# Optimization experiments

Hardware: AMD Instinct MI355X
Metric: run time of the kernel (lower is better)

The kernel has to match this reference:

```python
import jax, jax.numpy as jnp
import numpy as np

B, L, D, H = 4, 1024, 1024, 16
HD = D // H
TERM = 20  # N-term / C-term window size


def setup_inputs() -> dict:
    key = jax.random.key(0)
    ks = jax.random.split(key, 9)
    x = jax.random.normal(ks[0], (B, L, D), jnp.float32)
    lens = jax.random.randint(ks[1], (B,), 64, L + 1)
    mask = jnp.arange(L)[None, :] < lens[:, None]  # contiguous valid prefix, bool [B,L]
    s = 0.02  # ~ xavier_uniform with gain 1/H**0.25
    Wq = jax.random.normal(ks[2], (D, D), jnp.float32) * s
    Wk = jax.random.normal(ks[3], (D, D), jnp.float32) * s
    Wv = jax.random.normal(ks[4], (D, D), jnp.float32) * s
    bq = jnp.zeros((D,), jnp.float32)
    bk = jnp.zeros((D,), jnp.float32)
    bv = jnp.zeros((D,), jnp.float32)
    gamma = jnp.ones((D,), jnp.float32)
    beta = jnp.zeros((D,), jnp.float32)
    return {"x": x, "mask": mask, "Wq": Wq, "bq": bq, "Wk": Wk, "bk": bk,
            "Wv": Wv, "bv": bv, "gamma": gamma, "beta": beta}


def reference(x, mask, Wq, bq, Wk, bk, Wv, bv, gamma, beta):
    # LayerNorm (eps = 1e-5, torch default)
    mu = x.mean(-1, keepdims=True)
    var = ((x - mu) ** 2).mean(-1, keepdims=True)
    xn = (x - mu) / jnp.sqrt(var + 1e-5) * gamma + beta

    Q = (xn @ Wq + bq).reshape(B, L, H, HD)
    K = (xn @ Wk + bk).reshape(B, L, H, HD)
    V = (xn @ Wv + bv).reshape(B, L, H, HD)

    # note: original divides by head_dim**0.25 (quarter power) - keep faithful
    scores = jnp.einsum('bqhd,bkhd->bhqk', Q, K) / HD ** 0.25

    # mask fill on key positions
    scores = jnp.where(mask[:, None, None, :], scores, -10000.0)

    # per-sample length-dependent bias on key positions
    lens = mask.sum(-1)                      # [B] int
    pos = jnp.arange(L)                      # [L]
    inlen = pos[None, :] < lens[:, None]     # [B,L]
    bias_ge = (1.0 * (pos[None, :] < TERM)
               + 0.8 * ((pos[None, :] >= lens[:, None] - TERM) & inlen))
    bias_lt = (1.0 + 0.8) * inlen
    bias = jnp.where((lens >= TERM)[:, None], bias_ge, bias_lt)  # [B,L]
    scores = scores + bias[:, None, None, :]

    attn = jax.nn.softmax(scores, axis=-1)   # [B,H,L,L]
    entropy_loss = -(attn * jnp.log(attn + 1e-10)).sum(-1).mean()

    context = jnp.einsum('bhqk,bkhd->bqhd', attn, V).reshape(B, L, D)

    # ragged N-term / C-term mean pooling (vectorized segment means)
    term = jnp.minimum(TERM, lens)           # [B]
    termf = term.astype(x.dtype)[:, None]
    wn = (pos[None, :] < term[:, None]).astype(x.dtype)                      # first term tokens
    wc = ((pos[None, :] >= (lens - term)[:, None]) & inlen).astype(x.dtype)  # last term valid tokens
    n_term = (context * wn[:, :, None]).sum(1) / termf
    c_term = (context * wc[:, :, None]).sum(1) / termf
    global_pool = context.mean(1)            # mean over full L, as in original

    pooled = jnp.concatenate([n_term, c_term, global_pool], axis=1)  # [B,3D]
    return pooled, attn.mean(1), entropy_loss
```

## Files before the change

kernel.cpp:

```cpp
#include <hip/hip_runtime.h>
#include <hip/hip_bf16.h>
#include <hip/hip_fp16.h>


typedef unsigned short u16;
typedef __attribute__((ext_vector_type(4))) float f32x4;
typedef __attribute__((ext_vector_type(8))) __bf16 bf16x8;
typedef __attribute__((ext_vector_type(4))) unsigned int u32x4;
typedef __attribute__((ext_vector_type(4))) unsigned short u16x4;
typedef __attribute__((ext_vector_type(8))) unsigned short u16x8;

typedef const __attribute__((address_space(1))) unsigned int* gas1;
typedef __attribute__((address_space(3))) unsigned int* las3;

#define DEV __device__ __forceinline__

DEV float bf2f(u16 u){ union{unsigned i; float f;} c; c.i = ((unsigned)u)<<16; return c.f; }
DEV u16 f2bf(float f){ union{float f; unsigned i;} c; c.f=f; unsigned i=c.i;
  unsigned r = i + 0x7FFFu + ((i>>16)&1u); return (u16)(r>>16); }

__global__ void k_detect(const void* mask, const void* gamma, const void* beta,
                         const void* bq, const void* bk, const void* bv,
                         int* lens, float* ent, int* flag,
                         u16* gam_c, u16* bet_c, u16* bq_c, u16* bk_c, u16* bv_c,
                         float* pacc){
  int t = threadIdx.x; int w = t>>6; int lane = t&63;
  int isf32 = (((const u16*)gamma)[0] == 0) ? 1 : 0;
  if (t==0){ *flag = isf32; *ent = 0.f; }
  for (int i=t; i<12288; i+=256) pacc[i] = 0.f;
  for (int i=t; i<1024; i+=256){
    if (isf32){
      gam_c[i]=f2bf(((const float*)gamma)[i]); bet_c[i]=f2bf(((const float*)beta)[i]);
      bq_c[i] =f2bf(((const float*)bq)[i]);    bk_c[i] =f2bf(((const float*)bk)[i]);
      bv_c[i] =f2bf(((const float*)bv)[i]);
    } else {
      gam_c[i]=((const u16*)gamma)[i]; bet_c[i]=((const u16*)beta)[i];
      bq_c[i] =((const u16*)bq)[i];    bk_c[i] =((const u16*)bk)[i];
      bv_c[i] =((const u16*)bv)[i];
    }
  }
  const unsigned char* mb = (const unsigned char*)mask;
  const int* mi = (const int*)mask;
  const u16* ms = (const u16*)mask;
  int cnt = 0;
  if (mb[1] != 0) {
    if (mb[0]==1 && mb[1]==1) { for (int i=lane;i<1024;i+=64) cnt += (mb[w*1024+i]!=0); }
    else                      { for (int i=lane;i<1024;i+=64) cnt += (ms[w*1024+i]!=0); }
  } else {
    if (mi[1]==0)             { for (int i=lane;i<1024;i+=64) cnt += (mi[(w*1024+i)*2]!=0); }
    else                      { for (int i=lane;i<1024;i+=64) cnt += (mi[w*1024+i]!=0); }
  }
  #pragma unroll
  for (int o=32;o;o>>=1) cnt += __shfl_down(cnt,o);
  if (lane==0) lens[w] = cnt;
}

__global__ __launch_bounds__(256) void k_ln(const void* x, const u16* gamma, const u16* beta,
                                            u16* xn, const int* flagp){
  int isf32 = *flagp;
  int row = blockIdx.x, t = threadIdx.x;
  float f0,f1,f2,f3;
  if (isf32){
    f32x4 v = ((const f32x4*)x)[(size_t)row*256 + t];
    f0=v[0]; f1=v[1]; f2=v[2]; f3=v[3];
  } else {
    u16x4 v = ((const u16x4*)x)[(size_t)row*256 + t];
    f0=bf2f(v[0]); f1=bf2f(v[1]); f2=bf2f(v[2]); f3=bf2f(v[3]);
  }
  float s = f0+f1+f2+f3;
  float sq = f0*f0+f1*f1+f2*f2+f3*f3;
  #pragma unroll
  for (int o=32;o;o>>=1){ s += __shfl_down(s,o); sq += __shfl_down(sq,o); }
  __shared__ float rs[4], rq[4];
  if ((t&63)==0){ rs[t>>6]=s; rq[t>>6]=sq; }
  __syncthreads();
  s = rs[0]+rs[1]+rs[2]+rs[3]; sq = rq[0]+rq[1]+rq[2]+rq[3];
  float mu = s*(1.0f/1024.0f);
  float var = sq*(1.0f/1024.0f) - mu*mu;
  float rstd = rsqrtf(var + 1e-5f);
  u16x4 gv = ((const u16x4*)gamma)[t];
  u16x4 bv = ((const u16x4*)beta)[t];
  u16x4 o;
  o[0]=f2bf((f0-mu)*rstd*bf2f(gv[0])+bf2f(bv[0]));
  o[1]=f2bf((f1-mu)*rstd*bf2f(gv[1])+bf2f(bv[1]));
  o[2]=f2bf((f2-mu)*rstd*bf2f(gv[2])+bf2f(bv[2]));
  o[3]=f2bf((f3-mu)*rstd*bf2f(gv[3])+bf2f(bv[3]));
  ((u16x4*)(xn + (size_t)row*1024))[t] = o;
}

DEV void tr64_body(const void* src, u16* dst, int R, int C, int bt, int isf32, int t,
                   u16 (*tile)[68]){
  int tc_n = C>>6;
  int tr = (bt / tc_n)<<6, tc = (bt % tc_n)<<6;
  if (isf32){
    const float* s = (const float*)src;
    #pragma unroll
    for (int it=0; it<2; ++it){
      int f = it*2048 + t*8; int r=f>>6, c=f&63;
      const float* p = s + (long)(tr+r)*C + tc + c;
      f32x4 a = *(const f32x4*)p, b = *(const f32x4*)(p+4);
      u16x4 ua, ub;
      #pragma unroll
      for (int j=0;j<4;j++){ ua[j]=f2bf(a[j]); ub[j]=f2bf(b[j]); }
      *(u16x4*)&tile[r][c]   = ua;
      *(u16x4*)&tile[r][c+4] = ub;
    }
  } else {
    const u16* s = (const u16*)src;
    #pragma unroll
    for (int it=0; it<2; ++it){
      int f = it*2048 + t*8; int r=f>>6, c=f&63;
      *(u16x4*)&tile[r][c]   = *(const u16x4*)(s + (long)(tr+r)*C + tc + c);
      *(u16x4*)&tile[r][c+4] = *(const u16x4*)(s + (long)(tr+r)*C + tc + c + 4);
    }
  }
  __syncthreads();
  #pragma unroll
  for (int it=0; it<2; ++it){
    int f = it*2048 + t*8; int r=f>>6, c=f&63;
    u16x4 a, b2;
    #pragma unroll
    for (int j=0;j<4;j++){ a[j]=tile[c+j][r]; b2[j]=tile[c+4+j][r]; }
    *(u16x4*)(dst + (long)(tc+r)*R + tr + c)     = a;
    *(u16x4*)(dst + (long)(tc+r)*R + tr + c + 4) = b2;
  }
}

__global__ __launch_bounds__(256) void k_trW(const void* Wq, const void* Wk, const void* Wv,
                                             u16* Wt, const int* flagp){
  __shared__ u16 tile[64][68];
  int isf32 = *flagp;
  const void* src = (blockIdx.y==0) ? Wq : (blockIdx.y==1) ? Wk : Wv;
  u16* dst = Wt + ((size_t)blockIdx.y<<20);
  tr64_body(src, dst, 1024, 1024, blockIdx.x, isf32, threadIdx.x, tile);
}

__global__ __launch_bounds__(256) void k_trV(const u16* Vb, u16* Vt){
  __shared__ u16 tile[64][68];
  tr64_body(Vb + ((size_t)blockIdx.y<<16), Vt + ((size_t)blockIdx.y<<16),
            1024, 64, blockIdx.x, 0, threadIdx.x, tile);
}

__global__ __launch_bounds__(256) void k_gemm(const u16* A, const u16* Bt,
    const u16* biasq, const u16* biask, const u16* biasv,
    u16* Qb, u16* Kb, u16* Vb){
  __shared__ u16 lA[2][4096];
  __shared__ u16 lB[2][4096];
  int t = threadIdx.x;
  int w = t>>6, l = t&63, g = l>>4, lc = l&15;
  int wm = w>>1, wn = w&1;
  int m0 = (blockIdx.x & 31)<<7;
  int n0 = (int)(blockIdx.x >> 5)<<7;
  int fb0 = t*16, fb1 = 4096 + t*16;
  int r0 = fb0>>6, c0 = fb0&63, r1 = fb1>>6, c1 = fb1&63;
  const char* Ab = (const char*)A; const char* Bb = (const char*)Bt;
  long aoff0 = (long)(m0+r0)*2048 + c0;
  long aoff1 = (long)(m0+r1)*2048 + c1;
  long boff0 = (long)(n0+r0)*2048 + c0;
  long boff1 = (long)(n0+r1)*2048 + c1;
  int lw = w<<10;

  #define STAGEK(buf, ko) do{ \
    __builtin_amdgcn_global_load_lds((gas1)(const void*)(Ab + aoff0 + (ko)), \
        (las3)(void*)((char*)&lA[buf][0] + lw), 16, 0, 0); \
    __builtin_amdgcn_global_load_lds((gas1)(const void*)(Ab + aoff1 + (ko)), \
        (las3)(void*)((char*)&lA[buf][0] + 4096 + lw), 16, 0, 0); \
    __builtin_amdgcn_global_load_lds((gas1)(const void*)(Bb + boff0 + (ko)), \
        (las3)(void*)((char*)&lB[buf][0] + lw), 16, 0, 0); \
    __builtin_amdgcn_global_load_lds((gas1)(const void*)(Bb + boff1 + (ko)), \
        (las3)(void*)((char*)&lB[buf][0] + 4096 + lw), 16, 0, 0); \
  }while(0)

  f32x4 vzero = {0.f,0.f,0.f,0.f};
  f32x4 acc[4][4];
  #pragma unroll
  for (int i=0;i<4;i++)
    #pragma unroll
    for (int j=0;j<4;j++) acc[i][j] = vzero;

  STAGEK(0, 0);
  __syncthreads();
  for (int kt=0; kt<32; ++kt){
    int cur = kt & 1;
    if (kt < 31) STAGEK(cur^1, (long)(kt+1)*64);
    bf16x8 af[4], bfr[4];
    #pragma unroll
    for (int i=0;i<4;i++) af[i]  = *(const bf16x8*)(const void*)&lA[cur][((wm<<6)+(i<<4)+lc)*32 + (g<<3)];
    #pragma unroll
    for (int j=0;j<4;j++) bfr[j] = *(const bf16x8*)(const void*)&lB[cur][((wn<<6)+(j<<4)+lc)*32 + (g<<3)];
    #pragma unroll
    for (int i=0;i<4;i++)
      #pragma unroll
      for (int j=0;j<4;j++)
        acc[i][j] = __builtin_amdgcn_mfma_f32_16x16x32_bf16(af[i], bfr[j], acc[i][j], 0,0,0);
    __syncthreads();
  }
  #undef STAGEK
  #pragma unroll
  for (int j=0;j<4;j++){
    int n = n0 + (wn<<6) + (j<<4) + lc;
    int kind = n>>10; int nn = n & 1023;
    const u16* bp = (kind==0)?biasq:(kind==1)?biask:biasv;
    float bvl = bf2f(bp[nn]);
    u16* dst = (kind==0)?Qb:(kind==1)?Kb:Vb;
    int h = nn>>6, hd = n&63;
    #pragma unroll
    for (int i=0;i<4;i++){
      #pragma unroll
      for (int r=0;r<4;r++){
        int m = m0 + (wm<<6) + (i<<4) + (g<<2) + r;
        int bb = m>>10, pos = m&1023;
        dst[(((bb<<4)+h)<<16) + (pos<<6) + hd] = f2bf(acc[i][j][r] + bvl);
      }
    }
  }
}

__global__ __launch_bounds__(512) void k_attn(const u16* Qg, const u16* Kg, const u16* Vt,
    const int* lens, u16* ctx, u16* Pp, float* ent_acc){
  __shared__ u16 Plds[16][1032];
  __shared__ float redz[16][8];
  __shared__ float rede[16][8];
  __shared__ __half redc[2][16][66];
  int bqi = blockIdx.x;
  int qt = bqi & 63, hg = (bqi>>6)&3, b = bqi>>8;
  int q0 = qt<<4;
  int t = threadIdx.x, w = t>>6, l = t&63, g = l>>4, lc = l&15;
  int kh = w>>2, dg = w&3;
  int len = lens[b];
  {
    u16x8 z8 = {0,0,0,0,0,0,0,0};
    u16* pz = &Plds[0][0];
    for (int i=t; i<2064; i+=512) *(u16x8*)(pz + i*8) = z8;
  }
  __half2 mh[8][2];
  #pragma unroll
  for (int i=0;i<8;i++){ mh[i][0] = __float2half2_rn(0.f); mh[i][1] = __float2half2_rn(0.f); }
  float ent_local = 0.f;
  const float SCALE = 0.35355339059327373f;
  for (int hh=0; hh<4; ++hh){
    int h = (hg<<2) + hh;
    int base = ((b<<4)+h)<<16;
    bf16x8 qf0 = *(const bf16x8*)(const void*)(Qg + base + ((q0+lc)<<6) + (g<<3));
    bf16x8 qf1 = *(const bf16x8*)(const void*)(Qg + base + ((q0+lc)<<6) + (g<<3) + 32);
    f32x4 s[8];
    float zp[4]={0,0,0,0}, ep[4]={0,0,0,0};
    #pragma unroll
    for (int tt=0; tt<8; ++tt){
      int kb = (tt<<7)+(w<<4);
      if (kb < len){
        const u16* kp = Kg + base + ((kb+lc)<<6) + (g<<3);
        bf16x8 kf0 = *(const bf16x8*)(const void*)kp;
        bf16x8 kf1 = *(const bf16x8*)(const void*)(kp + 32);
        f32x4 a = {0.f,0.f,0.f,0.f};
        a = __builtin_amdgcn_mfma_f32_16x16x32_bf16(qf0, kf0, a, 0,0,0);
        a = __builtin_amdgcn_mfma_f32_16x16x32_bf16(qf1, kf1, a, 0,0,0);
        int key = kb + lc;
        bool valid = key < len;
        float bias;
        if (len >= 20) bias = (key<20 ? 1.0f : 0.0f) + ((valid && key >= len-20) ? 0.8f : 0.0f);
        else bias = 1.8f;
        #pragma unroll
        for (int r=0;r<4;r++){
          float sv = valid ? a[r]*SCALE + bias : -10000.0f;
          float e = __expf(fminf(sv, 60.0f));
          zp[r]+=e; ep[r]+=e*sv;
          a[r] = e;
          Plds[(g<<2)+r][key] = f2bf(e);
        }
        s[tt] = a;
      }
    }
    #pragma unroll
    for (int r=0;r<4;r++){
      zp[r]+=__shfl_xor(zp[r],1); ep[r]+=__shfl_xor(ep[r],1);
      zp[r]+=__shfl_xor(zp[r],2); ep[r]+=__shfl_xor(ep[r],2);
      zp[r]+=__shfl_xor(zp[r],4); ep[r]+=__shfl_xor(ep[r],4);
      zp[r]+=__shfl_xor(zp[r],8); ep[r]+=__shfl_xor(ep[r],8);
    }
    if (lc==0){
      #pragma unroll
      for (int r=0;r<4;r++){ redz[(g<<2)+r][w]=zp[r]; rede[(g<<2)+r][w]=ep[r]; }
    }
    __syncthreads();
    float invz[4];
    #pragma unroll
    for (int r=0;r<4;r++){
      int rr=(g<<2)+r;
      float Z = redz[rr][0]+redz[rr][1]+redz[rr][2]+redz[rr][3]
              + redz[rr][4]+redz[rr][5]+redz[rr][6]+redz[rr][7];
      float E = rede[rr][0]+rede[rr][1]+rede[rr][2]+rede[rr][3]
              + rede[rr][4]+rede[rr][5]+rede[rr][6]+rede[rr][7];
      invz[r] = 1.0f/Z;
      if (w==0 && lc==0) ent_local += __logf(Z) - E*invz[r];
    }
    #pragma unroll
    for (int tt=0;tt<8;++tt){
      if (((tt<<7)+(w<<4)) < len){
        float p0 = s[tt][0]*invz[0], p1 = s[tt][1]*invz[1];
        float p2 = s[tt][2]*invz[2], p3 = s[tt][3]*invz[3];
        mh[tt][0] = __hadd2(mh[tt][0], __halves2half2(__float2half_rn(p0), __float2half_rn(p1)));
        mh[tt][1] = __hadd2(mh[tt][1], __halves2half2(__float2half_rn(p2), __float2half_rn(p3)));
      }
    }
    f32x4 cacc = {0.f,0.f,0.f,0.f};
    const u16* vrow = Vt + base + (((dg<<4)+lc)<<10);
    #pragma unroll
    for (int ks=0; ks<16; ++ks){
      int kk = (ks<<1)+kh;
      if ((kk<<5) < len){
        bf16x8 pa = *(const bf16x8*)(const void*)(&Plds[0][0] + lc*1032 + (kk<<5) + (g<<3));
        bf16x8 vb = *(const bf16x8*)(const void*)(vrow + (kk<<5) + (g<<3));
        cacc = __builtin_amdgcn_mfma_f32_16x16x32_bf16(pa, vb, cacc, 0,0,0);
      }
    }
    #pragma unroll
    for (int r=0;r<4;r++) redc[kh][(g<<2)+r][(dg<<4)+lc] = __float2half(cacc[r]*invz[r]);
    __syncthreads();
    #pragma unroll
    for (int ii=0; ii<2; ++ii){
      int i = t + (ii<<9);
      int q = i>>6, d = i&63;
      float v = __half2float(redc[0][q][d]) + __half2float(redc[1][q][d]);
      ctx[(((size_t)(b<<10)+q0+q)<<10) + (h<<6) + d] = f2bf(v);
    }
  }
  u16* oa = Pp + ((size_t)hg<<22) + ((size_t)b<<20);
  #pragma unroll
  for (int tt=0; tt<8; ++tt){
    int col = (tt<<7)+(w<<4)+lc;
    int qb_ = (q0+(g<<2))<<10;
    oa[qb_ + col]            = __half_as_ushort(__low2half(mh[tt][0]));
    oa[qb_ + 1024 + col]     = __half_as_ushort(__high2half(mh[tt][0]));
    oa[qb_ + 2048 + col]     = __half_as_ushort(__low2half(mh[tt][1]));
    oa[qb_ + 3072 + col]     = __half_as_ushort(__high2half(mh[tt][1]));
  }
  if (w==0){
    float es = ent_local;
    #pragma unroll
    for (int o=32;o;o>>=1) es += __shfl_down(es,o);
    if (l==0) atomicAdd(ent_acc, es);
  }
}

__global__ __launch_bounds__(256) void k_pmean(const u16* Pp, void* out_v, const int* flagp){
  int isf32 = *flagp;
  size_t idx = ((size_t)blockIdx.x*256 + threadIdx.x)*8;
  int b = (int)(idx>>20); size_t f = idx & 0xFFFFFu;
  const u16* p0 = Pp + ((size_t)b<<20) + f;
  float s[8] = {0,0,0,0,0,0,0,0};
  #pragma unroll
  for (int gI=0; gI<4; ++gI){
    u16x8 v = *(const u16x8*)(p0 + ((size_t)gI<<22));
    #pragma unroll
    for (int j=0;j<8;j++) s[j] += __half2float(__ushort_as_half(v[j]));
  }
  if (isf32){
    float* o = (float*)out_v + 12288 + idx;
    #pragma unroll
    for (int j=0;j<8;j++) o[j] = s[j]*0.0625f;
  } else {
    u16x8 o;
    #pragma unroll
    for (int j=0;j<8;j++) o[j] = f2bf(s[j]*0.0625f);
    *(u16x8*)((u16*)out_v + 12288 + idx) = o;
  }
}

__global__ __launch_bounds__(256) void k_pool1(const u16* ctx, const int* lens, float* pacc){
  int b = blockIdx.y, pc = blockIdx.x;
  int t = threadIdx.x; int d0 = t*4;
  int len = lens[b];
  int term = len < 20 ? len : 20;
  int lo = len - term;
  float sn[4]={0,0,0,0}, sc[4]={0,0,0,0}, sg[4]={0,0,0,0};
  const u16* base = ctx + ((size_t)b<<20) + ((size_t)pc<<15) + d0;
  for (int p=0;p<32;++p){
    int gp = (pc<<5)+p;
    u16x4 v = *(const u16x4*)(base + ((size_t)p<<10));
    bool in_n = gp < term;
    bool in_c = (gp >= lo) && (gp < len);
    #pragma unroll
    for (int j=0;j<4;j++){
      float fv = bf2f(v[j]);
      sg[j] += fv;
      if (in_n) sn[j] += fv;
      if (in_c) sc[j] += fv;
    }
  }
  #pragma unroll
  for (int j=0;j<4;j++){
    atomicAdd(&pacc[(b<<10)+d0+j], sn[j]);
    atomicAdd(&pacc[4096+(b<<10)+d0+j], sc[j]);
    atomicAdd(&pacc[8192+(b<<10)+d0+j], sg[j]);
  }
}

__global__ __launch_bounds__(256) void k_pool2(const float* pacc, const int* lens, const float* ent,
                                               void* out_v, const int* flagp){
  int isf32 = *flagp;
  int idx = blockIdx.x*256 + threadIdx.x;
  if (idx < 12288){
    int b = idx/3072; int r = idx - b*3072; int seg = r>>10; int d = r&1023;
    int len = lens[b]; int term = len < 20 ? len : 20;
    float scale = (seg==2) ? (1.0f/1024.0f) : (1.0f/(float)term);
    float v = pacc[seg*4096 + (b<<10) + d]*scale;
    if (isf32) ((float*)out_v)[idx] = v; else ((u16*)out_v)[idx] = f2bf(v);
  }
  if (idx==0){
    float e = (*ent)*(1.0f/65536.0f);
    if (isf32) ((float*)out_v)[4206592] = e; else ((u16*)out_v)[4206592] = f2bf(e);
  }
}

extern "C" void kernel_launch(void* const* d_in, const int* in_sizes, int n_in,
                              void* d_out, int out_size, void* d_ws, size_t ws_size,
                              hipStream_t stream){
  (void)in_sizes; (void)n_in; (void)out_size; (void)ws_size;
  const void* x     = d_in[0];
  const void* mask  = d_in[1];
  const void* Wq    = d_in[2];
  const void* bq    = d_in[3];
  const void* Wk    = d_in[4];
  const void* bk    = d_in[5];
  const void* Wv    = d_in[6];
  const void* bv    = d_in[7];
  const void* gamma = d_in[8];
  const void* beta  = d_in[9];

  char* ws = (char*)d_ws;
  int*   lens = (int*)ws;
  float* ent  = (float*)(ws + 64);
  int*   flag = (int*)(ws + 68);
  u16* gam_c = (u16*)(ws + 256);
  u16* bet_c = gam_c + 1024;
  u16* bq_c  = bet_c + 1024;
  u16* bk_c  = bq_c + 1024;
  u16* bv_c  = bk_c + 1024;
  u16* xn  = (u16*)(ws + 0x100000);
  u16* Qb  = (u16*)(ws + 0x900000);
  u16* Kb  = (u16*)(ws + 0x1100000);
  u16* ctx = (u16*)(ws + 0x1900000);
  u16* Pp  = (u16*)(ws + 0x2100000);
  u16* Wt  = (u16*)(ws + 0x2100000);
  u16* Vb  = (u16*)(ws + 0x2700000);
  u16* Vt  = xn;
  float* pacc = (float*)(ws + 0x4100000);

  k_detect<<<1,256,0,stream>>>(mask, gamma, beta, bq, bk, bv,
                               lens, ent, flag, gam_c, bet_c, bq_c, bk_c, bv_c, pacc);
  k_ln<<<4096,256,0,stream>>>(x, gam_c, bet_c, xn, flag);
  k_trW<<<dim3(256,3),256,0,stream>>>(Wq, Wk, Wv, Wt, flag);
  k_gemm<<<768,256,0,stream>>>(xn, Wt, bq_c, bk_c, bv_c, Qb, Kb, Vb);
  k_trV<<<dim3(16,64),256,0,stream>>>(Vb, Vt);
  k_attn<<<1024,512,0,stream>>>(Qb, Kb, Vt, lens, ctx, Pp, ent);
  k_pmean<<<2048,256,0,stream>>>(Pp, d_out, flag);
  k_pool1<<<dim3(32,4),256,0,stream>>>(ctx, lens, pacc);
  k_pool2<<<49,256,0,stream>>>(pacc, lens, ent, d_out, flag);
}
```

Before: 170.8 us.

## Skip K/V GEMM tiles for padded rows and merge small kernels

GEMM tiles that produce K or V for rows past a sample's valid length now return early. Those keys are masked to -10000 before the softmax, so their values should not affect the output. LayerNorm and the weight transpose are merged into one launch, as are the probability-mean and pooling kernels, to cut launch count and let the independent work overlap. The risk is that the skipped K/V rows keep stale workspace contents; if those are non-finite they could leak into results through 0*inf.

```diff
diff --git a/kernel.cpp b/kernel.cpp
--- a/kernel.cpp
+++ b/kernel.cpp
@@ -55,39 +55,6 @@
   if (lane==0) lens[w] = cnt;
 }
 
-__global__ __launch_bounds__(256) void k_ln(const void* x, const u16* gamma, const u16* beta,
-                                            u16* xn, const int* flagp){
-  int isf32 = *flagp;
-  int row = blockIdx.x, t = threadIdx.x;
-  float f0,f1,f2,f3;
-  if (isf32){
-    f32x4 v = ((const f32x4*)x)[(size_t)row*256 + t];
-    f0=v[0]; f1=v[1]; f2=v[2]; f3=v[3];
-  } else {
-    u16x4 v = ((const u16x4*)x)[(size_t)row*256 + t];
-    f0=bf2f(v[0]); f1=bf2f(v[1]); f2=bf2f(v[2]); f3=bf2f(v[3]);
-  }
-  float s = f0+f1+f2+f3;
-  float sq = f0*f0+f1*f1+f2*f2+f3*f3;
-  #pragma unroll
-  for (int o=32;o;o>>=1){ s += __shfl_down(s,o); sq += __shfl_down(sq,o); }
-  __shared__ float rs[4], rq[4];
-  if ((t&63)==0){ rs[t>>6]=s; rq[t>>6]=sq; }
-  __syncthreads();
-  s = rs[0]+rs[1]+rs[2]+rs[3]; sq = rq[0]+rq[1]+rq[2]+rq[3];
-  float mu = s*(1.0f/1024.0f);
-  float var = sq*(1.0f/1024.0f) - mu*mu;
-  float rstd = rsqrtf(var + 1e-5f);
-  u16x4 gv = ((const u16x4*)gamma)[t];
-  u16x4 bv = ((const u16x4*)beta)[t];
-  u16x4 o;
-  o[0]=f2bf((f0-mu)*rstd*bf2f(gv[0])+bf2f(bv[0]));
-  o[1]=f2bf((f1-mu)*rstd*bf2f(gv[1])+bf2f(bv[1]));
-  o[2]=f2bf((f2-mu)*rstd*bf2f(gv[2])+bf2f(bv[2]));
-  o[3]=f2bf((f3-mu)*rstd*bf2f(gv[3])+bf2f(bv[3]));
-  ((u16x4*)(xn + (size_t)row*1024))[t] = o;
-}
-
 DEV void tr64_body(const void* src, u16* dst, int R, int C, int bt, int isf32, int t,
                    u16 (*tile)[68]){
   int tc_n = C>>6;
@@ -126,13 +93,47 @@
   }
 }
 
-__global__ __launch_bounds__(256) void k_trW(const void* Wq, const void* Wk, const void* Wv,
-                                             u16* Wt, const int* flagp){
+__global__ __launch_bounds__(256) void k_prep(const void* x, const u16* gamma, const u16* beta,
+    u16* xn, const void* Wq, const void* Wk, const void* Wv, u16* Wt, const int* flagp){
   __shared__ u16 tile[64][68];
   int isf32 = *flagp;
-  const void* src = (blockIdx.y==0) ? Wq : (blockIdx.y==1) ? Wk : Wv;
-  u16* dst = Wt + ((size_t)blockIdx.y<<20);
-  tr64_body(src, dst, 1024, 1024, blockIdx.x, isf32, threadIdx.x, tile);
+  int id = blockIdx.x, t = threadIdx.x;
+  if (id < 4096){
+    int row = id;
+    float f0,f1,f2,f3;
+    if (isf32){
+      f32x4 v = ((const f32x4*)x)[(size_t)row*256 + t];
+      f0=v[0]; f1=v[1]; f2=v[2]; f3=v[3];
+    } else {
+      u16x4 v = ((const u16x4*)x)[(size_t)row*256 + t];
+      f0=bf2f(v[0]); f1=bf2f(v[1]); f2=bf2f(v[2]); f3=bf2f(v[3]);
+    }
+    float s = f0+f1+f2+f3;
+    float sq = f0*f0+f1*f1+f2*f2+f3*f3;
+    #pragma unroll
+    for (int o=32;o;o>>=1){ s += __shfl_down(s,o); sq += __shfl_down(sq,o); }
+    float* rs = (float*)&tile[0][0];
+    float* rq = rs + 4;
+    if ((t&63)==0){ rs[t>>6]=s; rq[t>>6]=sq; }
+    __syncthreads();
+    s = rs[0]+rs[1]+rs[2]+rs[3]; sq = rq[0]+rq[1]+rq[2]+rq[3];
+    float mu = s*(1.0f/1024.0f);
+    float var = sq*(1.0f/1024.0f) - mu*mu;
+    float rstd = rsqrtf(var + 1e-5f);
+    u16x4 gv = ((const u16x4*)gamma)[t];
+    u16x4 bv = ((const u16x4*)beta)[t];
+    u16x4 o;
+    o[0]=f2bf((f0-mu)*rstd*bf2f(gv[0])+bf2f(bv[0]));
+    o[1]=f2bf((f1-mu)*rstd*bf2f(gv[1])+bf2f(bv[1]));
+    o[2]=f2bf((f2-mu)*rstd*bf2f(gv[2])+bf2f(bv[2]));
+    o[3]=f2bf((f3-mu)*rstd*bf2f(gv[3])+bf2f(bv[3]));
+    ((u16x4*)(xn + (size_t)row*1024))[t] = o;
+  } else {
+    int bt = id - 4096;
+    int sub = bt >> 8, tl = bt & 255;
+    const void* src = (sub==0) ? Wq : (sub==1) ? Wk : Wv;
+    tr64_body(src, Wt + ((size_t)sub<<20), 1024, 1024, tl, isf32, t, tile);
+  }
 }
 
 __global__ __launch_bounds__(256) void k_trV(const u16* Vb, u16* Vt){
@@ -143,14 +144,15 @@
 
 __global__ __launch_bounds__(256) void k_gemm(const u16* A, const u16* Bt,
     const u16* biasq, const u16* biask, const u16* biasv,
-    u16* Qb, u16* Kb, u16* Vb){
+    u16* Qb, u16* Kb, u16* Vb, const int* lens){
+  int m0 = (blockIdx.x & 31)<<7;
+  int n0 = (int)(blockIdx.x >> 5)<<7;
+  if (n0 >= 1024 && (m0 & 1023) >= lens[m0>>10]) return;
   __shared__ u16 lA[2][4096];
   __shared__ u16 lB[2][4096];
   int t = threadIdx.x;
   int w = t>>6, l = t&63, g = l>>4, lc = l&15;
   int wm = w>>1, wn = w&1;
-  int m0 = (blockIdx.x & 31)<<7;
-  int n0 = (int)(blockIdx.x >> 5)<<7;
   int fb0 = t*16, fb1 = 4096 + t*16;
   int r0 = fb0>>6, c0 = fb0&63, r1 = fb1>>6, c1 = fb1&63;
   const char* Ab = (const char*)A; const char* Bb = (const char*)Bt;
@@ -343,56 +345,59 @@
   }
 }
 
-__global__ __launch_bounds__(256) void k_pmean(const u16* Pp, void* out_v, const int* flagp){
-  int isf32 = *flagp;
-  size_t idx = ((size_t)blockIdx.x*256 + threadIdx.x)*8;
-  int b = (int)(idx>>20); size_t f = idx & 0xFFFFFu;
-  const u16* p0 = Pp + ((size_t)b<<20) + f;
-  float s[8] = {0,0,0,0,0,0,0,0};
-  #pragma unroll
-  for (int gI=0; gI<4; ++gI){
-    u16x8 v = *(const u16x8*)(p0 + ((size_t)gI<<22));
-    #pragma unroll
-    for (int j=0;j<8;j++) s[j] += __half2float(__ushort_as_half(v[j]));
-  }
-  if (isf32){
-    float* o = (float*)out_v + 12288 + idx;
-    #pragma unroll
-    for (int j=0;j<8;j++) o[j] = s[j]*0.0625f;
+__global__ __launch_bounds__(256) void k_pmix(const u16* Pp, void* out_v, const int* flagp,
+                                              const u16* ctx, const int* lens, float* pacc){
+  int id = blockIdx.x;
+  if (id < 2048){
+    int isf32 = *flagp;
+    size_t idx = ((size_t)id*256 + threadIdx.x)*8;
+    int b = (int)(idx>>20); size_t f = idx & 0xFFFFFu;
+    const u16* p0 = Pp + ((size_t)b<<20) + f;
+    float s[8] = {0,0,0,0,0,0,0,0};
+    #pragma unroll
+    for (int gI=0; gI<4; ++gI){
+      u16x8 v = *(const u16x8*)(p0 + ((size_t)gI<<22));
+      #pragma unroll
+      for (int j=0;j<8;j++) s[j] += __half2float(__ushort_as_half(v[j]));
+    }
+    if (isf32){
+      float* o = (float*)out_v + 12288 + idx;
+      #pragma unroll
+      for (int j=0;j<8;j++) o[j] = s[j]*0.0625f;
+    } else {
+      u16x8 o;
+      #pragma unroll
+      for (int j=0;j<8;j++) o[j] = f2bf(s[j]*0.0625f);
+      *(u16x8*)((u16*)out_v + 12288 + idx) = o;
+    }
   } else {
-    u16x8 o;
-    #pragma unroll
-    for (int j=0;j<8;j++) o[j] = f2bf(s[j]*0.0625f);
-    *(u16x8*)((u16*)out_v + 12288 + idx) = o;
-  }
-}
-
-__global__ __launch_bounds__(256) void k_pool1(const u16* ctx, const int* lens, float* pacc){
-  int b = blockIdx.y, pc = blockIdx.x;
-  int t = threadIdx.x; int d0 = t*4;
-  int len = lens[b];
-  int term = len < 20 ? len : 20;
-  int lo = len - term;
-  float sn[4]={0,0,0,0}, sc[4]={0,0,0,0}, sg[4]={0,0,0,0};
-  const u16* base = ctx + ((size_t)b<<20) + ((size_t)pc<<15) + d0;
-  for (int p=0;p<32;++p){
-    int gp = (pc<<5)+p;
-    u16x4 v = *(const u16x4*)(base + ((size_t)p<<10));
-    bool in_n = gp < term;
-    bool in_c = (gp >= lo) && (gp < len);
+    int pid = id - 2048;
+    int b = pid>>5, pc = pid&31;
+    int t = threadIdx.x; int d0 = t*4;
+    int len = lens[b];
+    int term = len < 20 ? len : 20;
+    int lo = len - term;
+    float sn[4]={0,0,0,0}, sc[4]={0,0,0,0}, sg[4]={0,0,0,0};
+    const u16* base = ctx + ((size_t)b<<20) + ((size_t)pc<<15) + d0;
+    for (int p=0;p<32;++p){
+      int gp = (pc<<5)+p;
+      u16x4 v = *(const u16x4*)(base + ((size_t)p<<10));
+      bool in_n = gp < term;
+      bool in_c = (gp >= lo) && (gp < len);
+      #pragma unroll
+      for (int j=0;j<4;j++){
+        float fv = bf2f(v[j]);
+        sg[j] += fv;
+        if (in_n) sn[j] += fv;
+        if (in_c) sc[j] += fv;
+      }
+    }
     #pragma unroll
     for (int j=0;j<4;j++){
-      float fv = bf2f(v[j]);
-      sg[j] += fv;
-      if (in_n) sn[j] += fv;
-      if (in_c) sc[j] += fv;
-    }
-  }
-  #pragma unroll
-  for (int j=0;j<4;j++){
-    atomicAdd(&pacc[(b<<10)+d0+j], sn[j]);
-    atomicAdd(&pacc[4096+(b<<10)+d0+j], sc[j]);
-    atomicAdd(&pacc[8192+(b<<10)+d0+j], sg[j]);
+      atomicAdd(&pacc[(b<<10)+d0+j], sn[j]);
+      atomicAdd(&pacc[4096+(b<<10)+d0+j], sc[j]);
+      atomicAdd(&pacc[8192+(b<<10)+d0+j], sg[j]);
+    }
   }
 }
 
@@ -449,12 +454,10 @@
 
   k_detect<<<1,256,0,stream>>>(mask, gamma, beta, bq, bk, bv,
                                lens, ent, flag, gam_c, bet_c, bq_c, bk_c, bv_c, pacc);
-  k_ln<<<4096,256,0,stream>>>(x, gam_c, bet_c, xn, flag);
-  k_trW<<<dim3(256,3),256,0,stream>>>(Wq, Wk, Wv, Wt, flag);
-  k_gemm<<<768,256,0,stream>>>(xn, Wt, bq_c, bk_c, bv_c, Qb, Kb, Vb);
+  k_prep<<<4864,256,0,stream>>>(x, gam_c, bet_c, xn, Wq, Wk, Wv, Wt, flag);
+  k_gemm<<<768,256,0,stream>>>(xn, Wt, bq_c, bk_c, bv_c, Qb, Kb, Vb, lens);
   k_trV<<<dim3(16,64),256,0,stream>>>(Vb, Vt);
   k_attn<<<1024,512,0,stream>>>(Qb, Kb, Vt, lens, ctx, Pp, ent);
-  k_pmean<<<2048,256,0,stream>>>(Pp, d_out, flag);
-  k_pool1<<<dim3(32,4),256,0,stream>>>(ctx, lens, pacc);
+  k_pmix<<<2176,256,0,stream>>>(Pp, d_out, flag, ctx, lens, pacc);
   k_pool2<<<49,256,0,stream>>>(pacc, lens, ent, d_out, flag);
 }
```

Measured after the change: 165.3 us (median of 3 runs). 1.03x faster.
